# Optimization experiments

Measured on AMD Instinct MI355X. Metric: run time of the kernel, lower is better.

## Reference

```python
import jax, jax.numpy as jnp
import numpy as np

NUM_NODES = 100000
NUM_EDGES = 1600000
FEAT = 128
HID = 128
NUM_GRAPHS = 512


def setup_inputs() -> dict:
    key = jax.random.key(0)
    ks = jax.random.split(key, 8)
    x = jax.random.normal(ks[0], (NUM_NODES, FEAT), dtype=jnp.float32)
    edge_index = jax.random.randint(ks[1], (2, NUM_EDGES), 0, NUM_NODES, dtype=jnp.int64)
    batch = jnp.sort(jax.random.randint(ks[2], (NUM_NODES,), 0, NUM_GRAPHS, dtype=jnp.int64))
    # Glorot-ish init for weights (scale named for clarity)
    s1 = 1.0 / np.sqrt(FEAT)
    s2 = 1.0 / np.sqrt(HID)
    W1 = jax.random.normal(ks[3], (FEAT, HID), dtype=jnp.float32) * s1
    b1 = jnp.zeros((HID,), dtype=jnp.float32)
    W2 = jax.random.normal(ks[4], (HID, HID), dtype=jnp.float32) * s2
    b2 = jnp.zeros((HID,), dtype=jnp.float32)
    Wout = jax.random.normal(ks[5], (HID, 1), dtype=jnp.float32) * s2
    bout = jnp.zeros((1,), dtype=jnp.float32)
    return {"x": x, "edge_index": edge_index, "batch": batch,
            "W1": W1, "b1": b1, "W2": W2, "b2": b2, "Wout": Wout, "bout": bout}


def reference(x, edge_index, batch, W1, b1, W2, b2, Wout, bout):
    N = x.shape[0]
    # PyG GCNConv: add self-loops, symmetric normalization D^-1/2 (A+I) D^-1/2
    loops = jnp.arange(N, dtype=edge_index.dtype)
    src = jnp.concatenate([edge_index[0], loops])  # [E+N]
    dst = jnp.concatenate([edge_index[1], loops])  # [E+N]
    ones = jnp.ones_like(dst, dtype=x.dtype)
    deg = jax.ops.segment_sum(ones, dst, num_segments=N)  # in-degree incl. self-loop
    dinv = jnp.where(deg > 0, jax.lax.rsqrt(deg), 0.0)
    coeff = (dinv[src] * dinv[dst])[:, None]  # [E+N, 1]

    def gcn(h, W, b):
        h = h @ W                                       # [N, H] dense GEMM
        msg = h[src] * coeff                            # gather + scale
        agg = jax.ops.segment_sum(msg, dst, num_segments=N)  # scatter-add
        return agg + b

    h = jax.nn.relu(gcn(x, W1, b1))
    h = jax.nn.relu(gcn(h, W2, b2))

    # global_mean_pool over batch ids
    G = NUM_GRAPHS
    sums = jax.ops.segment_sum(h, batch, num_segments=G)
    cnts = jax.ops.segment_sum(jnp.ones((N,), dtype=h.dtype), batch, num_segments=G)
    pooled = sums / jnp.maximum(cnts, 1.0)[:, None]

    return pooled @ Wout + bout  # [G, 1]
```

## Files before the change

kernel.cpp:

```cpp
#include <hip/hip_runtime.h>
#include <hip/hip_bf16.h>
#include <hip/hip_fp16.h>

#define FEAT 128
#define PSLOTS 64
#define BSH 7
#define BNODES 128
#define BCAP 2560
#define NBIN 512

typedef _Float16 h8 __attribute__((ext_vector_type(8)));
typedef float f4 __attribute__((ext_vector_type(4)));
typedef float fx2 __attribute__((ext_vector_type(2)));


__device__ __forceinline__ void wt_body(const float* __restrict__ W1,
                                        const float* __restrict__ W2,
                                        __half* __restrict__ Wt1,
                                        __half* __restrict__ Wt2, int bid) {
    int t = bid * 256 + threadIdx.x;
    const float* W = (t < 8192) ? W1 : W2;
    __half* Wt     = (t < 8192) ? Wt1 : Wt2;
    int u = t & 8191;
    int n = u >> 6, k2 = (u & 63) * 2;
    float a = W[(size_t)k2 * 128 + n];
    float b = W[(size_t)(k2 + 1) * 128 + n];
    ((__half2*)Wt)[n * 64 + (k2 >> 1)] = __floats2half2_rn(a, b);
}

__device__ __forceinline__ void bin_body(const int* __restrict__ ei, int E, int chunk,
                                         int* __restrict__ cursor,
                                         unsigned* __restrict__ binned, int nb,
                                         int bid, int* smem) {
    int* hist = smem;
    int* base = smem + 1024;
    int start = bid * chunk;
    int end = start + chunk; if (end > E) end = E;
    bool vec4 = ((E & 3) == 0);
    int end4 = vec4 ? (start + ((end - start) & ~3)) : start;

    for (int i = threadIdx.x; i < nb; i += 256) hist[i] = 0;
    __syncthreads();
    for (int e = start + threadIdx.x * 4; e < end4; e += 1024) {
        int4 d4 = *(const int4*)(ei + E + e);
        atomicAdd(&hist[d4.x >> BSH], 1);
        atomicAdd(&hist[d4.y >> BSH], 1);
        atomicAdd(&hist[d4.z >> BSH], 1);
        atomicAdd(&hist[d4.w >> BSH], 1);
    }
    for (int e = end4 + threadIdx.x; e < end; e += 256)
        atomicAdd(&hist[ei[E + e] >> BSH], 1);
    __syncthreads();
    for (int i = threadIdx.x; i < nb; i += 256) {
        int h = hist[i];
        base[i] = h ? atomicAdd(&cursor[i], h) : 0;
    }
    __syncthreads();
    for (int e = start + threadIdx.x * 4; e < end4; e += 1024) {
        int4 s4 = *(const int4*)(ei + e);
        int4 d4 = *(const int4*)(ei + E + e);
        int sv[4] = {s4.x, s4.y, s4.z, s4.w};
        int dv[4] = {d4.x, d4.y, d4.z, d4.w};
#pragma unroll
        for (int j = 0; j < 4; ++j) {
            int b = dv[j] >> BSH;
            int pos = atomicAdd(&base[b], 1);
            if (pos < BCAP)
                binned[(size_t)b * BCAP + pos] =
                    (unsigned)sv[j] | ((unsigned)(dv[j] & (BNODES - 1)) << 17);
        }
    }
    for (int e = end4 + threadIdx.x; e < end; e += 256) {
        int s = ei[e];
        int d = ei[E + e];
        int b = d >> BSH;
        int pos = atomicAdd(&base[b], 1);
        if (pos < BCAP)
            binned[(size_t)b * BCAP + pos] =
                (unsigned)s | ((unsigned)(d & (BNODES - 1)) << 17);
    }
}

__global__ __launch_bounds__(256) void bin_wt(const int* __restrict__ ei, int E, int chunk,
                                              int* __restrict__ cursor,
                                              unsigned* __restrict__ binned, int nb,
                                              const float* __restrict__ W1,
                                              const float* __restrict__ W2,
                                              __half* __restrict__ Wt1,
                                              __half* __restrict__ Wt2) {
    __shared__ int smem[2048];
    if ((int)blockIdx.x < NBIN)
        bin_body(ei, E, chunk, cursor, binned, nb, blockIdx.x, smem);
    else
        wt_body(W1, W2, Wt1, Wt2, blockIdx.x - NBIN);
}


__device__ __forceinline__ void stage_wt(const __half* __restrict__ Wt, _Float16* Bs) {
    const float4* src = (const float4*)Wt;
    float4* dst = (float4*)Bs;
    for (int i = threadIdx.x; i < 2048; i += 256) {
        int n = i >> 4, ch = i & 15;
        dst[n * 16 + (ch ^ (n & 15))] = src[i];
    }
}

__device__ __forceinline__ void loadA(const __half* p, int quad, h8* a) {
#pragma unroll
    for (int ks = 0; ks < 4; ++ks)
        a[ks] = *(const h8*)(p + ks * 32 + quad * 8);
}
__device__ __forceinline__ void loadA(const float* p, int quad, h8* a) {
#pragma unroll
    for (int ks = 0; ks < 4; ++ks) {
        const float* q = p + ks * 32 + quad * 8;
        float4 f0 = *(const float4*)q;
        float4 f1 = *(const float4*)(q + 4);
        h8 v;
        v[0] = (_Float16)f0.x; v[1] = (_Float16)f0.y;
        v[2] = (_Float16)f0.z; v[3] = (_Float16)f0.w;
        v[4] = (_Float16)f1.x; v[5] = (_Float16)f1.y;
        v[6] = (_Float16)f1.z; v[7] = (_Float16)f1.w;
        a[ks] = v;
    }
}

template <typename TIN>
__device__ __forceinline__ void gemm_tile(const TIN* __restrict__ X, const _Float16* Bs,
                                          int rowb, int N, int m, int quad,
                                          f4 acc[2][8]) {
    h8 a[2][4];
#pragma unroll
    for (int rt = 0; rt < 2; ++rt) {
        int rA = rowb + rt * 64 + m; if (rA >= N) rA = N - 1;
        loadA(X + (size_t)rA * FEAT, quad, a[rt]);
    }
#pragma unroll
    for (int rt = 0; rt < 2; ++rt)
#pragma unroll
        for (int nt = 0; nt < 8; ++nt) acc[rt][nt] = (f4){0.f, 0.f, 0.f, 0.f};
#pragma unroll
    for (int nt = 0; nt < 8; ++nt) {
        const _Float16* bbase = Bs + (nt * 16 + m) * 128;
#pragma unroll
        for (int ks = 0; ks < 4; ++ks) {
            int ch = (ks * 4 + quad) ^ m;
            h8 bfrag = *(const h8*)(bbase + ch * 8);
            acc[0][nt] = __builtin_amdgcn_mfma_f32_16x16x32_f16(a[0][ks], bfrag, acc[0][nt], 0, 0, 0);
            acc[1][nt] = __builtin_amdgcn_mfma_f32_16x16x32_f16(a[1][ks], bfrag, acc[1][nt], 0, 0, 0);
        }
    }
}


__global__ __launch_bounds__(256) void k_build1(const unsigned* __restrict__ binned,
                                                const int* __restrict__ cursor,
                                                const float* __restrict__ X,
                                                const __half* __restrict__ Wt1,
                                                int N, int* __restrict__ deg,
                                                int* __restrict__ rowstart,
                                                int* __restrict__ meta,
                                                unsigned char* __restrict__ Y) {
    __shared__ __align__(16) _Float16 Bs[128 * 128];
    __shared__ int ld[256];
    __shared__ int sc[256];
    __shared__ int cur[256];
    int b = blockIdx.x;

    stage_wt(Wt1, Bs);

    int cnt = cursor[b]; if (cnt > BCAP) cnt = BCAP;
    int s = b * BCAP, e = s + cnt;
    ld[threadIdx.x] = 0;
    __syncthreads();
    for (int i = s + threadIdx.x; i < e; i += 256)
        atomicAdd(&ld[binned[i] >> 17], 1);
    __syncthreads();
    int d = ld[threadIdx.x];
    sc[threadIdx.x] = d;
    __syncthreads();
    for (int off = 1; off < 256; off <<= 1) {
        int t = (threadIdx.x >= off) ? sc[threadIdx.x - off] : 0;
        __syncthreads();
        sc[threadIdx.x] += t;
        __syncthreads();
    }
    int rs = s + sc[threadIdx.x] - d;
    cur[threadIdx.x] = rs;
    int v = (b << BSH) + threadIdx.x;
    if (threadIdx.x < BNODES && v < N) {
        deg[v] = d;
        rowstart[v] = rs;
    }
    __syncthreads();
    for (int i = s + threadIdx.x; i < e; i += 256) {
        unsigned p = binned[i];
        int src = (int)(p & 0x1FFFF);
        int drl = (int)(p >> 17);
        int pos = atomicAdd(&cur[drl], 1);
        meta[pos] = src << 7;
    }

    int lane = threadIdx.x & 63;
    int wave = threadIdx.x >> 6;
    int m = lane & 15;
    int quad = lane >> 4;
    int rowb = (b << BSH) + wave * 16;
    f4 acc[2][8];
    gemm_tile<float>(X, Bs, rowb, N, m, quad, acc);
#pragma unroll
    for (int rt = 0; rt < 2; ++rt)
#pragma unroll
    for (int r = 0; r < 4; ++r) {
        int row = rowb + rt * 64 + quad * 4 + r;
        if (row < N) {
            float scv = rsqrtf((float)ld[row & (BNODES - 1)] + 1.0f);
#pragma unroll
            for (int nt = 0; nt < 8; ++nt) {
                float val = scv * acc[rt][nt][r];
                int pk = __builtin_amdgcn_cvt_pk_fp8_f32(val, val, 0, false);
                Y[(size_t)row * FEAT + nt * 16 + m] = (unsigned char)(pk & 0xFF);
            }
        }
    }
}


__global__ __launch_bounds__(256) void gemm_mfma(const __half* __restrict__ X,
                                                 const __half* __restrict__ Wt,
                                                 unsigned char* __restrict__ Y,
                                                 const int* __restrict__ deg, int N) {
    __shared__ __align__(16) _Float16 Bs[128 * 128];
    stage_wt(Wt, Bs);
    __syncthreads();
    int lane = threadIdx.x & 63;
    int wave = threadIdx.x >> 6;
    int m = lane & 15;
    int quad = lane >> 4;
    int rowb = blockIdx.x * 128 + wave * 16;
    f4 acc[2][8];
    gemm_tile<__half>(X, Bs, rowb, N, m, quad, acc);
#pragma unroll
    for (int rt = 0; rt < 2; ++rt)
#pragma unroll
    for (int r = 0; r < 4; ++r) {
        int row = rowb + rt * 64 + quad * 4 + r;
        if (row < N) {
            float scv = rsqrtf((float)deg[row] + 1.0f);
#pragma unroll
            for (int nt = 0; nt < 8; ++nt) {
                float val = scv * acc[rt][nt][r];
                int pk = __builtin_amdgcn_cvt_pk_fp8_f32(val, val, 0, false);
                Y[(size_t)row * FEAT + nt * 16 + m] = (unsigned char)(pk & 0xFF);
            }
        }
    }
}


__device__ __forceinline__ void accum8(uint2 u, fx2* acc) {
    acc[0] += __builtin_amdgcn_cvt_pk_f32_fp8((int)u.x, false);
    acc[1] += __builtin_amdgcn_cvt_pk_f32_fp8((int)u.x, true);
    acc[2] += __builtin_amdgcn_cvt_pk_f32_fp8((int)u.y, false);
    acc[3] += __builtin_amdgcn_cvt_pk_f32_fp8((int)u.y, true);
}

template <bool POOL>
__global__ __launch_bounds__(256) void agg_relu(const unsigned char* __restrict__ Y,
                                                const int* __restrict__ rowstart,
                                                const int* __restrict__ degc,
                                                const int* __restrict__ meta,
                                                const float* __restrict__ bias,
                                                __half* __restrict__ H, int N, int zoff,
                                                const float* __restrict__ Wout,
                                                const int* __restrict__ batch,
                                                float* __restrict__ gsum, int G) {
    int wid  = (blockIdx.x * 256 + threadIdx.x) >> 6;
    int lane = threadIdx.x & 63;
    if (wid >= N) return;
    int v = wid;
    int g = lane >> 4;
    int c = lane & 15;
    int cb = c * 8;
    const char* Ycb = (const char*)Y + cb;

    fx2 acc[4];
#pragma unroll
    for (int k = 0; k < 4; ++k) acc[k] = (fx2){0.f, 0.f};

    {
        int so = (g == 0) ? (v << 7) : zoff;
        uint2 u = *(const uint2*)(Ycb + so);
        accum8(u, acc);
    }

    int base = rowstart[v];
    int n = degc[v];
    int g4 = g * 4;
    for (int i0 = 0; i0 < n; i0 += 16) {
        int o[4];
#pragma unroll
        for (int j = 0; j < 4; ++j) {
            int idx = i0 + g4 + j;
            int mj = meta[base + idx];
            o[j] = (idx < n) ? mj : zoff;
        }
        uint2 u[4];
#pragma unroll
        for (int j = 0; j < 4; ++j)
            u[j] = *(const uint2*)(Ycb + o[j]);
#pragma unroll
        for (int j = 0; j < 4; ++j) accum8(u[j], acc);
    }

#pragma unroll
    for (int k = 0; k < 4; ++k) {
        fx2 t;
        t[0] = __shfl_xor(acc[k][0], 16);
        t[1] = __shfl_xor(acc[k][1], 16);
        acc[k] += t;
        t[0] = __shfl_xor(acc[k][0], 32);
        t[1] = __shfl_xor(acc[k][1], 32);
        acc[k] += t;
    }
    float dv = rsqrtf((float)n + 1.0f);

    if (POOL) {
        const float4* bp = (const float4*)(bias + cb);
        float4 b0 = bp[0], b1 = bp[1];
        const float4* wp = (const float4*)(Wout + cb);
        float4 w0 = wp[0], w1 = wp[1];
        float h0 = fmaxf(dv * acc[0][0] + b0.x, 0.f);
        float h1 = fmaxf(dv * acc[0][1] + b0.y, 0.f);
        float h2 = fmaxf(dv * acc[1][0] + b0.z, 0.f);
        float h3 = fmaxf(dv * acc[1][1] + b0.w, 0.f);
        float h4 = fmaxf(dv * acc[2][0] + b1.x, 0.f);
        float h5 = fmaxf(dv * acc[2][1] + b1.y, 0.f);
        float h6 = fmaxf(dv * acc[3][0] + b1.z, 0.f);
        float h7 = fmaxf(dv * acc[3][1] + b1.w, 0.f);
        float s = h0 * w0.x + h1 * w0.y + h2 * w0.z + h3 * w0.w
                + h4 * w1.x + h5 * w1.y + h6 * w1.z + h7 * w1.w;
        if (g == 0) {
            s += __shfl_xor(s, 1);
            s += __shfl_xor(s, 2);
            s += __shfl_xor(s, 4);
            s += __shfl_xor(s, 8);
            if (lane == 0) {
                int slot = blockIdx.x & (PSLOTS - 1);
                atomicAdd(&gsum[slot * G + batch[v]], s);
            }
        }
    } else {
        fx2 av;
        if (g == 0)      av = acc[0];
        else if (g == 1) av = acc[1];
        else if (g == 2) av = acc[2];
        else             av = acc[3];
        float2 bb = *(const float2*)(bias + cb + g * 2);
        float hx = fmaxf(dv * av[0] + bb.x, 0.f);
        float hy = fmaxf(dv * av[1] + bb.y, 0.f);
        *(__half2*)(H + (size_t)v * FEAT + cb + g * 2) = __floats2half2_rn(hx, hy);
    }
}


__global__ __launch_bounds__(256) void k_head(const float* __restrict__ gsum,
                                              const int* __restrict__ batch, int N, int G,
                                              const float* __restrict__ bout,
                                              float* __restrict__ out) {
    int g = blockIdx.x * 256 + threadIdx.x;
    if (g >= G) return;
    float s = 0.f;
#pragma unroll 8
    for (int k = 0; k < PSLOTS; ++k) s += gsum[k * G + g];
    int lo = 0, hi = N;
    while (lo < hi) { int mid = (lo + hi) >> 1; if (batch[mid] < g) lo = mid + 1; else hi = mid; }
    int start = lo;
    lo = start; hi = N;
    while (lo < hi) { int mid = (lo + hi) >> 1; if (batch[mid] < g + 1) lo = mid + 1; else hi = mid; }
    int cnt = lo - start;
    out[g] = s / (float)(cnt > 0 ? cnt : 1) + bout[0];
}


extern "C" void kernel_launch(void* const* d_in, const int* in_sizes, int n_in,
                              void* d_out, int out_size, void* d_ws, size_t ws_size,
                              hipStream_t stream) {
    const float* x    = (const float*)d_in[0];
    const int*   ei   = (const int*)d_in[1];
    const int*   batch= (const int*)d_in[2];
    const float* W1   = (const float*)d_in[3];
    const float* b1   = (const float*)d_in[4];
    const float* W2   = (const float*)d_in[5];
    const float* b2   = (const float*)d_in[6];
    const float* Wout = (const float*)d_in[7];
    const float* bout = (const float*)d_in[8];

    int N = in_sizes[0] / FEAT;
    int E = in_sizes[1] / 2;
    int G = out_size;
    int nb = (N + BNODES - 1) >> BSH;

    char* ws = (char*)d_ws;
    size_t off = 0;
    auto alloc = [&](size_t bytes) -> void* {
        void* p = ws + off;
        off += (bytes + 255) & ~(size_t)255;
        return p;
    };
    unsigned char* bufY = (unsigned char*)alloc((size_t)N * FEAT);
    __half* bufH     = (__half*)alloc((size_t)N * FEAT * 2);
    __half* Wt1      = (__half*)alloc((size_t)FEAT * FEAT * 2);
    __half* Wt2      = (__half*)alloc((size_t)FEAT * FEAT * 2);
    size_t zbytes    = 256 + (size_t)PSLOTS * G * 4 + (size_t)nb * 4;
    char*  zr        = (char*)alloc(zbytes);
    unsigned char* padrow = (unsigned char*)zr;
    float* gsum      = (float*)(zr + 256);
    int*   cursor    = (int*)(gsum + (size_t)PSLOTS * G);
    int    zoff      = (int)((char*)padrow - (char*)bufY);
    int*   deg       = (int*)alloc((size_t)N * 4);
    int*   rowstart  = (int*)alloc((size_t)N * 4);
    unsigned* binned = (unsigned*)alloc((size_t)nb * BCAP * 4);
    int*   meta      = (int*)alloc(((size_t)nb * BCAP + 64) * 4);

    int gemm_grid = (N + 127) / 128;
    int agg_grid  = (N + 3) / 4;
    int chunkB = (((E + NBIN - 1) / NBIN) + 3) & ~3;

    hipMemsetAsync(zr, 0, zbytes, stream);
    bin_wt<<<NBIN + 64, 256, 0, stream>>>(ei, E, chunkB, cursor, binned, nb,
                                          W1, W2, Wt1, Wt2);
    k_build1<<<nb, 256, 0, stream>>>(binned, cursor, x, Wt1, N, deg, rowstart, meta, bufY);
    agg_relu<false><<<agg_grid, 256, 0, stream>>>(bufY, rowstart, deg, meta, b1, bufH, N, zoff,
                                                  nullptr, nullptr, nullptr, 0);
    gemm_mfma<<<gemm_grid, 256, 0, stream>>>(bufH, Wt2, bufY, deg, N);
    agg_relu<true><<<agg_grid, 256, 0, stream>>>(bufY, rowstart, deg, meta, b2, nullptr, N, zoff,
                                                 Wout, batch, gsum, G);
    k_head<<<(G + 255) / 256, 256, 0, stream>>>(gsum, batch, N, G, bout, (float*)d_out);
}
```

Baseline: 277.7 us.

## Run layer-1 GEMM concurrently with edge binning, apply source norm in aggregation

The first-layer GEMM no longer waits for the degree computation. It writes unscaled fp8 rows and runs in the same launch as the edge-binning blocks, so the dense and sparse setup work overlap. The source-side normalization moves into the first aggregation as a per-edge weight gathered from a new dinv array. The memset and weight transpose are folded into one init kernel. The cost is an extra per-edge dinv gather and multiply in layer 1, plus the fp8 quantization now applying to unscaled values.

Result: slower. 286.1 us (+3.1%).

```diff
diff --git a/kernel.cpp b/kernel.cpp
--- a/kernel.cpp
+++ b/kernel.cpp
@@ -28,6 +28,18 @@
     ((__half2*)Wt)[n * 64 + (k2 >> 1)] = __floats2half2_rn(a, b);
 }
 
+
+__global__ __launch_bounds__(256) void k_init(const float* __restrict__ W1,
+                                              const float* __restrict__ W2,
+                                              __half* __restrict__ Wt1,
+                                              __half* __restrict__ Wt2,
+                                              uint4* __restrict__ zr, int zwords) {
+    if ((int)blockIdx.x < 64) { wt_body(W1, W2, Wt1, Wt2, blockIdx.x); return; }
+    int t = (blockIdx.x - 64) * 256 + threadIdx.x;
+    int stride = (gridDim.x - 64) * 256;
+    for (int i = t; i < zwords; i += stride) zr[i] = make_uint4(0, 0, 0, 0);
+}
+
 __device__ __forceinline__ void bin_body(const int* __restrict__ ei, int E, int chunk,
                                          int* __restrict__ cursor,
                                          unsigned* __restrict__ binned, int nb,
@@ -81,20 +93,6 @@
     }
 }
 
-__global__ __launch_bounds__(256) void bin_wt(const int* __restrict__ ei, int E, int chunk,
-                                              int* __restrict__ cursor,
-                                              unsigned* __restrict__ binned, int nb,
-                                              const float* __restrict__ W1,
-                                              const float* __restrict__ W2,
-                                              __half* __restrict__ Wt1,
-                                              __half* __restrict__ Wt2) {
-    __shared__ int smem[2048];
-    if ((int)blockIdx.x < NBIN)
-        bin_body(ei, E, chunk, cursor, binned, nb, blockIdx.x, smem);
-    else
-        wt_body(W1, W2, Wt1, Wt2, blockIdx.x - NBIN);
-}
-
 
 __device__ __forceinline__ void stage_wt(const __half* __restrict__ Wt, _Float16* Bs) {
     const float4* src = (const float4*)Wt;
@@ -152,69 +150,17 @@
     }
 }
 
-
-__global__ __launch_bounds__(256) void k_build1(const unsigned* __restrict__ binned,
-                                                const int* __restrict__ cursor,
-                                                const float* __restrict__ X,
-                                                const __half* __restrict__ Wt1,
-                                                int N, int* __restrict__ deg,
-                                                int* __restrict__ rowstart,
-                                                int* __restrict__ meta,
-                                                unsigned char* __restrict__ Y) {
-    __shared__ __align__(16) _Float16 Bs[128 * 128];
-    __shared__ int ld[256];
-    __shared__ int sc[256];
-    __shared__ int cur[256];
-    int b = blockIdx.x;
-
-    stage_wt(Wt1, Bs);
-
-    int cnt = cursor[b]; if (cnt > BCAP) cnt = BCAP;
-    int s = b * BCAP, e = s + cnt;
-    ld[threadIdx.x] = 0;
-    __syncthreads();
-    for (int i = s + threadIdx.x; i < e; i += 256)
-        atomicAdd(&ld[binned[i] >> 17], 1);
-    __syncthreads();
-    int d = ld[threadIdx.x];
-    sc[threadIdx.x] = d;
-    __syncthreads();
-    for (int off = 1; off < 256; off <<= 1) {
-        int t = (threadIdx.x >= off) ? sc[threadIdx.x - off] : 0;
-        __syncthreads();
-        sc[threadIdx.x] += t;
-        __syncthreads();
-    }
-    int rs = s + sc[threadIdx.x] - d;
-    cur[threadIdx.x] = rs;
-    int v = (b << BSH) + threadIdx.x;
-    if (threadIdx.x < BNODES && v < N) {
-        deg[v] = d;
-        rowstart[v] = rs;
-    }
-    __syncthreads();
-    for (int i = s + threadIdx.x; i < e; i += 256) {
-        unsigned p = binned[i];
-        int src = (int)(p & 0x1FFFF);
-        int drl = (int)(p >> 17);
-        int pos = atomicAdd(&cur[drl], 1);
-        meta[pos] = src << 7;
-    }
-
-    int lane = threadIdx.x & 63;
-    int wave = threadIdx.x >> 6;
-    int m = lane & 15;
-    int quad = lane >> 4;
-    int rowb = (b << BSH) + wave * 16;
-    f4 acc[2][8];
-    gemm_tile<float>(X, Bs, rowb, N, m, quad, acc);
+template <bool SCALED>
+__device__ __forceinline__ void gemm_store(f4 acc[2][8], unsigned char* __restrict__ Y,
+                                           const int* __restrict__ deg,
+                                           int rowb, int N, int m, int quad) {
 #pragma unroll
     for (int rt = 0; rt < 2; ++rt)
 #pragma unroll
     for (int r = 0; r < 4; ++r) {
         int row = rowb + rt * 64 + quad * 4 + r;
         if (row < N) {
-            float scv = rsqrtf((float)ld[row & (BNODES - 1)] + 1.0f);
+            float scv = SCALED ? rsqrtf((float)deg[row] + 1.0f) : 1.0f;
 #pragma unroll
             for (int nt = 0; nt < 8; ++nt) {
                 float val = scv * acc[rt][nt][r];
@@ -222,6 +168,32 @@
                 Y[(size_t)row * FEAT + nt * 16 + m] = (unsigned char)(pk & 0xFF);
             }
         }
+    }
+}
+
+
+__global__ __launch_bounds__(256) void gemm_bin(const float* __restrict__ X,
+                                                const __half* __restrict__ Wt1,
+                                                unsigned char* __restrict__ Y, int N,
+                                                int gemm_grid,
+                                                const int* __restrict__ ei, int E, int chunk,
+                                                int* __restrict__ cursor,
+                                                unsigned* __restrict__ binned, int nb) {
+    __shared__ __align__(16) char smem[32768];
+    if ((int)blockIdx.x < gemm_grid) {
+        _Float16* Bs = (_Float16*)smem;
+        stage_wt(Wt1, Bs);
+        __syncthreads();
+        int lane = threadIdx.x & 63;
+        int wave = threadIdx.x >> 6;
+        int m = lane & 15;
+        int quad = lane >> 4;
+        int rowb = blockIdx.x * 128 + wave * 16;
+        f4 acc[2][8];
+        gemm_tile<float>(X, Bs, rowb, N, m, quad, acc);
+        gemm_store<false>(acc, Y, nullptr, rowb, N, m, quad);
+    } else {
+        bin_body(ei, E, chunk, cursor, binned, nb, blockIdx.x - gemm_grid, (int*)smem);
     }
 }
 
@@ -240,20 +212,51 @@
     int rowb = blockIdx.x * 128 + wave * 16;
     f4 acc[2][8];
     gemm_tile<__half>(X, Bs, rowb, N, m, quad, acc);
-#pragma unroll
-    for (int rt = 0; rt < 2; ++rt)
-#pragma unroll
-    for (int r = 0; r < 4; ++r) {
-        int row = rowb + rt * 64 + quad * 4 + r;
-        if (row < N) {
-            float scv = rsqrtf((float)deg[row] + 1.0f);
-#pragma unroll
-            for (int nt = 0; nt < 8; ++nt) {
-                float val = scv * acc[rt][nt][r];
-                int pk = __builtin_amdgcn_cvt_pk_fp8_f32(val, val, 0, false);
-                Y[(size_t)row * FEAT + nt * 16 + m] = (unsigned char)(pk & 0xFF);
-            }
-        }
+    gemm_store<true>(acc, Y, deg, rowb, N, m, quad);
+}
+
+
+__global__ __launch_bounds__(256) void k_build(const unsigned* __restrict__ binned,
+                                               const int* __restrict__ cursor,
+                                               int N, int* __restrict__ deg,
+                                               int* __restrict__ rowstart,
+                                               float* __restrict__ dinv,
+                                               int* __restrict__ meta) {
+    __shared__ int ld[256];
+    __shared__ int sc[256];
+    __shared__ int cur[256];
+    int b = blockIdx.x;
+    int cnt = cursor[b]; if (cnt > BCAP) cnt = BCAP;
+    int s = b * BCAP, e = s + cnt;
+    ld[threadIdx.x] = 0;
+    __syncthreads();
+    for (int i = s + threadIdx.x; i < e; i += 256)
+        atomicAdd(&ld[binned[i] >> 17], 1);
+    __syncthreads();
+    int d = ld[threadIdx.x];
+    sc[threadIdx.x] = d;
+    __syncthreads();
+    for (int off = 1; off < 256; off <<= 1) {
+        int t = (threadIdx.x >= off) ? sc[threadIdx.x - off] : 0;
+        __syncthreads();
+        sc[threadIdx.x] += t;
+        __syncthreads();
+    }
+    int rs = s + sc[threadIdx.x] - d;
+    cur[threadIdx.x] = rs;
+    int v = (b << BSH) + threadIdx.x;
+    if (threadIdx.x < BNODES && v < N) {
+        deg[v] = d;
+        rowstart[v] = rs;
+        dinv[v] = rsqrtf((float)d + 1.0f);
+    }
+    __syncthreads();
+    for (int i = s + threadIdx.x; i < e; i += 256) {
+        unsigned p = binned[i];
+        int src = (int)(p & 0x1FFFF);
+        int drl = (int)(p >> 17);
+        int pos = atomicAdd(&cur[drl], 1);
+        meta[pos] = src << 7;
     }
 }
 
@@ -264,11 +267,19 @@
     acc[2] += __builtin_amdgcn_cvt_pk_f32_fp8((int)u.y, false);
     acc[3] += __builtin_amdgcn_cvt_pk_f32_fp8((int)u.y, true);
 }
-
-template <bool POOL>
+__device__ __forceinline__ void accum8w(uint2 u, float cf, fx2* acc) {
+    fx2 c = (fx2){cf, cf};
+    acc[0] += c * __builtin_amdgcn_cvt_pk_f32_fp8((int)u.x, false);
+    acc[1] += c * __builtin_amdgcn_cvt_pk_f32_fp8((int)u.x, true);
+    acc[2] += c * __builtin_amdgcn_cvt_pk_f32_fp8((int)u.y, false);
+    acc[3] += c * __builtin_amdgcn_cvt_pk_f32_fp8((int)u.y, true);
+}
+
+template <bool POOL, bool WEIGHTED>
 __global__ __launch_bounds__(256) void agg_relu(const unsigned char* __restrict__ Y,
                                                 const int* __restrict__ rowstart,
                                                 const int* __restrict__ degc,
+                                                const float* __restrict__ dinv,
                                                 const int* __restrict__ meta,
                                                 const float* __restrict__ bias,
                                                 __half* __restrict__ H, int N, int zoff,
@@ -283,6 +294,7 @@
     int c = lane & 15;
     int cb = c * 8;
     const char* Ycb = (const char*)Y + cb;
+    float dv = WEIGHTED ? dinv[v] : 0.f;
 
     fx2 acc[4];
 #pragma unroll
@@ -291,7 +303,8 @@
     {
         int so = (g == 0) ? (v << 7) : zoff;
         uint2 u = *(const uint2*)(Ycb + so);
-        accum8(u, acc);
+        if (WEIGHTED) accum8w(u, dv, acc);
+        else          accum8(u, acc);
     }
 
     int base = rowstart[v];
@@ -299,18 +312,27 @@
     int g4 = g * 4;
     for (int i0 = 0; i0 < n; i0 += 16) {
         int o[4];
+        float cf[4];
 #pragma unroll
         for (int j = 0; j < 4; ++j) {
             int idx = i0 + g4 + j;
             int mj = meta[base + idx];
-            o[j] = (idx < n) ? mj : zoff;
+            bool ok = idx < n;
+            o[j] = ok ? mj : zoff;
+            if (WEIGHTED) {
+                cf[j] = 0.f;
+                if (ok) cf[j] = dinv[mj >> 7];
+            }
         }
         uint2 u[4];
 #pragma unroll
         for (int j = 0; j < 4; ++j)
             u[j] = *(const uint2*)(Ycb + o[j]);
 #pragma unroll
-        for (int j = 0; j < 4; ++j) accum8(u[j], acc);
+        for (int j = 0; j < 4; ++j) {
+            if (WEIGHTED) accum8w(u[j], cf[j], acc);
+            else          accum8(u[j], acc);
+        }
     }
 
 #pragma unroll
@@ -323,7 +345,7 @@
         t[1] = __shfl_xor(acc[k][1], 32);
         acc[k] += t;
     }
-    float dv = rsqrtf((float)n + 1.0f);
+    if (!WEIGHTED) dv = rsqrtf((float)n + 1.0f);
 
     if (POOL) {
         const float4* bp = (const float4*)(bias + cb);
@@ -420,21 +442,25 @@
     int    zoff      = (int)((char*)padrow - (char*)bufY);
     int*   deg       = (int*)alloc((size_t)N * 4);
     int*   rowstart  = (int*)alloc((size_t)N * 4);
+    float* dinv      = (float*)alloc((size_t)N * 4);
     unsigned* binned = (unsigned*)alloc((size_t)nb * BCAP * 4);
     int*   meta      = (int*)alloc(((size_t)nb * BCAP + 64) * 4);
 
     int gemm_grid = (N + 127) / 128;
     int agg_grid  = (N + 3) / 4;
     int chunkB = (((E + NBIN - 1) / NBIN) + 3) & ~3;
-
-    hipMemsetAsync(zr, 0, zbytes, stream);
-    bin_wt<<<NBIN + 64, 256, 0, stream>>>(ei, E, chunkB, cursor, binned, nb,
-                                          W1, W2, Wt1, Wt2);
-    k_build1<<<nb, 256, 0, stream>>>(binned, cursor, x, Wt1, N, deg, rowstart, meta, bufY);
-    agg_relu<false><<<agg_grid, 256, 0, stream>>>(bufY, rowstart, deg, meta, b1, bufH, N, zoff,
-                                                  nullptr, nullptr, nullptr, 0);
+    int zwords = (int)((zbytes + 15) / 16);
+
+    k_init<<<224, 256, 0, stream>>>(W1, W2, Wt1, Wt2, (uint4*)zr, zwords);
+    gemm_bin<<<gemm_grid + NBIN, 256, 0, stream>>>(x, Wt1, bufY, N, gemm_grid,
+                                                   ei, E, chunkB, cursor, binned, nb);
+    k_build<<<nb, 256, 0, stream>>>(binned, cursor, N, deg, rowstart, dinv, meta);
+    agg_relu<false, true><<<agg_grid, 256, 0, stream>>>(bufY, rowstart, deg, dinv, meta,
+                                                        b1, bufH, N, zoff,
+                                                        nullptr, nullptr, nullptr, 0);
     gemm_mfma<<<gemm_grid, 256, 0, stream>>>(bufH, Wt2, bufY, deg, N);
-    agg_relu<true><<<agg_grid, 256, 0, stream>>>(bufY, rowstart, deg, meta, b2, nullptr, N, zoff,
-                                                 Wout, batch, gsum, G);
+    agg_relu<true, false><<<agg_grid, 256, 0, stream>>>(bufY, rowstart, deg, dinv, meta,
+                                                        b2, nullptr, N, zoff,
+                                                        Wout, batch, gsum, G);
     k_head<<<(G + 255) / 256, 256, 0, stream>>>(gsum, batch, N, G, bout, (float*)d_out);
 }
```

## Fuse binning and build into persistent kernel with grid barrier; fold head into pool

Applied to the files above, without the earlier changes.

Merges the edge-binning/weight-transpose kernel and the per-bin CSR build + first GEMM into one persistent kernel of 768 blocks that synchronise through a global atomic spin barrier. The gsum zeroing also moves into that kernel, and the final head computation is folded into the last block of the pooling aggregation via a done counter. The aim is to cut launch gaps and the memset. In exchange it relies on all 768 blocks being co-resident for the spin barrier to be safe, and it serialises the head into a single block.

New measurement: 1.081 ms. 3.89x slower.

```diff
diff --git a/kernel.cpp b/kernel.cpp
--- a/kernel.cpp
+++ b/kernel.cpp
@@ -7,7 +7,8 @@
 #define BSH 7
 #define BNODES 128
 #define BCAP 2560
-#define NBIN 512
+#define NBIN 704
+#define KG_GRID 768
 
 typedef _Float16 h8 __attribute__((ext_vector_type(8)));
 typedef float f4 __attribute__((ext_vector_type(4)));
@@ -81,20 +82,6 @@
     }
 }
 
-__global__ __launch_bounds__(256) void bin_wt(const int* __restrict__ ei, int E, int chunk,
-                                              int* __restrict__ cursor,
-                                              unsigned* __restrict__ binned, int nb,
-                                              const float* __restrict__ W1,
-                                              const float* __restrict__ W2,
-                                              __half* __restrict__ Wt1,
-                                              __half* __restrict__ Wt2) {
-    __shared__ int smem[2048];
-    if ((int)blockIdx.x < NBIN)
-        bin_body(ei, E, chunk, cursor, binned, nb, blockIdx.x, smem);
-    else
-        wt_body(W1, W2, Wt1, Wt2, blockIdx.x - NBIN);
-}
-
 
 __device__ __forceinline__ void stage_wt(const __half* __restrict__ Wt, _Float16* Bs) {
     const float4* src = (const float4*)Wt;
@@ -153,20 +140,15 @@
 }
 
 
-__global__ __launch_bounds__(256) void k_build1(const unsigned* __restrict__ binned,
-                                                const int* __restrict__ cursor,
-                                                const float* __restrict__ X,
-                                                const __half* __restrict__ Wt1,
-                                                int N, int* __restrict__ deg,
-                                                int* __restrict__ rowstart,
-                                                int* __restrict__ meta,
-                                                unsigned char* __restrict__ Y) {
-    __shared__ __align__(16) _Float16 Bs[128 * 128];
-    __shared__ int ld[256];
-    __shared__ int sc[256];
-    __shared__ int cur[256];
-    int b = blockIdx.x;
-
+__device__ __forceinline__ void build_body(int b, const unsigned* __restrict__ binned,
+                                           const int* __restrict__ cursor,
+                                           const float* __restrict__ X,
+                                           const __half* __restrict__ Wt1,
+                                           int N, int* __restrict__ deg,
+                                           int* __restrict__ rowstart,
+                                           int* __restrict__ meta,
+                                           unsigned char* __restrict__ Y,
+                                           _Float16* Bs, int* ld, int* sc, int* cur) {
     stage_wt(Wt1, Bs);
 
     int cnt = cursor[b]; if (cnt > BCAP) cnt = BCAP;
@@ -226,6 +208,50 @@
 }
 
 
+__global__ __launch_bounds__(256, 4) void k_graph(const int* __restrict__ ei, int E, int chunk,
+                                                  int* __restrict__ cursor,
+                                                  unsigned* __restrict__ binned, int nb,
+                                                  const float* __restrict__ W1,
+                                                  const float* __restrict__ W2,
+                                                  __half* __restrict__ Wt1,
+                                                  __half* __restrict__ Wt2,
+                                                  uint4* __restrict__ zr4, int zwords,
+                                                  const float* __restrict__ X, int N,
+                                                  int* __restrict__ deg,
+                                                  int* __restrict__ rowstart,
+                                                  int* __restrict__ meta,
+                                                  unsigned char* __restrict__ Y,
+                                                  int* __restrict__ done1) {
+    __shared__ __align__(16) char smem[35840];
+    int u = blockIdx.x;
+    if (u < NBIN) {
+        bin_body(ei, E, chunk, cursor, binned, nb, u, (int*)smem);
+    } else {
+        int w = u - NBIN;
+        wt_body(W1, W2, Wt1, Wt2, w);
+        int i = w * 129 + (int)threadIdx.x;
+        if (threadIdx.x < 129 && i < zwords) zr4[i] = make_uint4(0, 0, 0, 0);
+    }
+    __syncthreads();
+    if (threadIdx.x == 0) {
+        __threadfence();
+        __hip_atomic_fetch_add(done1, 1, __ATOMIC_RELEASE, __HIP_MEMORY_SCOPE_AGENT);
+        while (__hip_atomic_load(done1, __ATOMIC_ACQUIRE, __HIP_MEMORY_SCOPE_AGENT) < (int)gridDim.x)
+            __builtin_amdgcn_s_sleep(2);
+        __threadfence();
+    }
+    __syncthreads();
+    _Float16* Bs = (_Float16*)smem;
+    int* ld = (int*)(smem + 32768);
+    int* sc = ld + 256;
+    int* cur = sc + 256;
+    for (int b = blockIdx.x; b < nb; b += gridDim.x) {
+        __syncthreads();
+        build_body(b, binned, cursor, X, Wt1, N, deg, rowstart, meta, Y, Bs, ld, sc, cur);
+    }
+}
+
+
 __global__ __launch_bounds__(256) void gemm_mfma(const __half* __restrict__ X,
                                                  const __half* __restrict__ Wt,
                                                  unsigned char* __restrict__ Y,
@@ -254,6 +280,26 @@
                 Y[(size_t)row * FEAT + nt * 16 + m] = (unsigned char)(pk & 0xFF);
             }
         }
+    }
+}
+
+
+__device__ void head_body(float* __restrict__ gsum, const int* __restrict__ batch,
+                          int N, int G, const float* __restrict__ bout,
+                          float* __restrict__ out) {
+    float bo = bout[0];
+    for (int g = threadIdx.x; g < G; g += 256) {
+        float s = 0.f;
+#pragma unroll 8
+        for (int k = 0; k < PSLOTS; ++k)
+            s += __hip_atomic_load(&gsum[k * G + g], __ATOMIC_RELAXED, __HIP_MEMORY_SCOPE_AGENT);
+        int lo = 0, hi = N;
+        while (lo < hi) { int mid = (lo + hi) >> 1; if (batch[mid] < g) lo = mid + 1; else hi = mid; }
+        int start = lo;
+        lo = start; hi = N;
+        while (lo < hi) { int mid = (lo + hi) >> 1; if (batch[mid] < g + 1) lo = mid + 1; else hi = mid; }
+        int cnt = lo - start;
+        out[g] = s / (float)(cnt > 0 ? cnt : 1) + bo;
     }
 }
 
@@ -274,112 +320,109 @@
                                                 __half* __restrict__ H, int N, int zoff,
                                                 const float* __restrict__ Wout,
                                                 const int* __restrict__ batch,
-                                                float* __restrict__ gsum, int G) {
+                                                float* __restrict__ gsum, int G,
+                                                int* __restrict__ done2,
+                                                const float* __restrict__ bout,
+                                                float* __restrict__ out) {
     int wid  = (blockIdx.x * 256 + threadIdx.x) >> 6;
     int lane = threadIdx.x & 63;
-    if (wid >= N) return;
-    int v = wid;
-    int g = lane >> 4;
-    int c = lane & 15;
-    int cb = c * 8;
-    const char* Ycb = (const char*)Y + cb;
-
-    fx2 acc[4];
-#pragma unroll
-    for (int k = 0; k < 4; ++k) acc[k] = (fx2){0.f, 0.f};
-
-    {
-        int so = (g == 0) ? (v << 7) : zoff;
-        uint2 u = *(const uint2*)(Ycb + so);
-        accum8(u, acc);
-    }
-
-    int base = rowstart[v];
-    int n = degc[v];
-    int g4 = g * 4;
-    for (int i0 = 0; i0 < n; i0 += 16) {
-        int o[4];
-#pragma unroll
-        for (int j = 0; j < 4; ++j) {
-            int idx = i0 + g4 + j;
-            int mj = meta[base + idx];
-            o[j] = (idx < n) ? mj : zoff;
-        }
-        uint2 u[4];
-#pragma unroll
-        for (int j = 0; j < 4; ++j)
-            u[j] = *(const uint2*)(Ycb + o[j]);
-#pragma unroll
-        for (int j = 0; j < 4; ++j) accum8(u[j], acc);
-    }
-
-#pragma unroll
-    for (int k = 0; k < 4; ++k) {
-        fx2 t;
-        t[0] = __shfl_xor(acc[k][0], 16);
-        t[1] = __shfl_xor(acc[k][1], 16);
-        acc[k] += t;
-        t[0] = __shfl_xor(acc[k][0], 32);
-        t[1] = __shfl_xor(acc[k][1], 32);
-        acc[k] += t;
-    }
-    float dv = rsqrtf((float)n + 1.0f);
-
+    bool active = wid < N;
+    if (active) {
+        int v = wid;
+        int g = lane >> 4;
+        int c = lane & 15;
+        int cb = c * 8;
+        const char* Ycb = (const char*)Y + cb;
+
+        fx2 acc[4];
+#pragma unroll
+        for (int k = 0; k < 4; ++k) acc[k] = (fx2){0.f, 0.f};
+
+        {
+            int so = (g == 0) ? (v << 7) : zoff;
+            uint2 u = *(const uint2*)(Ycb + so);
+            accum8(u, acc);
+        }
+
+        int base = rowstart[v];
+        int n = degc[v];
+        int g4 = g * 4;
+        for (int i0 = 0; i0 < n; i0 += 16) {
+            int o[4];
+#pragma unroll
+            for (int j = 0; j < 4; ++j) {
+                int idx = i0 + g4 + j;
+                int mj = meta[base + idx];
+                o[j] = (idx < n) ? mj : zoff;
+            }
+            uint2 u[4];
+#pragma unroll
+            for (int j = 0; j < 4; ++j)
+                u[j] = *(const uint2*)(Ycb + o[j]);
+#pragma unroll
+            for (int j = 0; j < 4; ++j) accum8(u[j], acc);
+        }
+
+#pragma unroll
+        for (int k = 0; k < 4; ++k) {
+            fx2 t;
+            t[0] = __shfl_xor(acc[k][0], 16);
+            t[1] = __shfl_xor(acc[k][1], 16);
+            acc[k] += t;
+            t[0] = __shfl_xor(acc[k][0], 32);
+            t[1] = __shfl_xor(acc[k][1], 32);
+            acc[k] += t;
+        }
+        float dv = rsqrtf((float)n + 1.0f);
+
+        if (POOL) {
+            const float4* bp = (const float4*)(bias + cb);
+            float4 b0 = bp[0], b1 = bp[1];
+            const float4* wp = (const float4*)(Wout + cb);
+            float4 w0 = wp[0], w1 = wp[1];
+            float h0 = fmaxf(dv * acc[0][0] + b0.x, 0.f);
+            float h1 = fmaxf(dv * acc[0][1] + b0.y, 0.f);
+            float h2 = fmaxf(dv * acc[1][0] + b0.z, 0.f);
+            float h3 = fmaxf(dv * acc[1][1] + b0.w, 0.f);
+            float h4 = fmaxf(dv * acc[2][0] + b1.x, 0.f);
+            float h5 = fmaxf(dv * acc[2][1] + b1.y, 0.f);
+            float h6 = fmaxf(dv * acc[3][0] + b1.z, 0.f);
+            float h7 = fmaxf(dv * acc[3][1] + b1.w, 0.f);
+            float s = h0 * w0.x + h1 * w0.y + h2 * w0.z + h3 * w0.w
+                    + h4 * w1.x + h5 * w1.y + h6 * w1.z + h7 * w1.w;
+            if (g == 0) {
+                s += __shfl_xor(s, 1);
+                s += __shfl_xor(s, 2);
+                s += __shfl_xor(s, 4);
+                s += __shfl_xor(s, 8);
+                if (lane == 0) {
+                    int slot = blockIdx.x & (PSLOTS - 1);
+                    atomicAdd(&gsum[slot * G + batch[wid]], s);
+                }
+            }
+        } else {
+            fx2 av;
+            if (g == 0)      av = acc[0];
+            else if (g == 1) av = acc[1];
+            else if (g == 2) av = acc[2];
+            else             av = acc[3];
+            float2 bb = *(const float2*)(bias + cb + g * 2);
+            float hx = fmaxf(dv * av[0] + bb.x, 0.f);
+            float hy = fmaxf(dv * av[1] + bb.y, 0.f);
+            *(__half2*)(H + (size_t)v * FEAT + cb + g * 2) = __floats2half2_rn(hx, hy);
+        }
+    }
     if (POOL) {
-        const float4* bp = (const float4*)(bias + cb);
-        float4 b0 = bp[0], b1 = bp[1];
-        const float4* wp = (const float4*)(Wout + cb);
-        float4 w0 = wp[0], w1 = wp[1];
-        float h0 = fmaxf(dv * acc[0][0] + b0.x, 0.f);
-        float h1 = fmaxf(dv * acc[0][1] + b0.y, 0.f);
-        float h2 = fmaxf(dv * acc[1][0] + b0.z, 0.f);
-        float h3 = fmaxf(dv * acc[1][1] + b0.w, 0.f);
-        float h4 = fmaxf(dv * acc[2][0] + b1.x, 0.f);
-        float h5 = fmaxf(dv * acc[2][1] + b1.y, 0.f);
-        float h6 = fmaxf(dv * acc[3][0] + b1.z, 0.f);
-        float h7 = fmaxf(dv * acc[3][1] + b1.w, 0.f);
-        float s = h0 * w0.x + h1 * w0.y + h2 * w0.z + h3 * w0.w
-                + h4 * w1.x + h5 * w1.y + h6 * w1.z + h7 * w1.w;
-        if (g == 0) {
-            s += __shfl_xor(s, 1);
-            s += __shfl_xor(s, 2);
-            s += __shfl_xor(s, 4);
-            s += __shfl_xor(s, 8);
-            if (lane == 0) {
-                int slot = blockIdx.x & (PSLOTS - 1);
-                atomicAdd(&gsum[slot * G + batch[v]], s);
-            }
-        }
-    } else {
-        fx2 av;
-        if (g == 0)      av = acc[0];
-        else if (g == 1) av = acc[1];
-        else if (g == 2) av = acc[2];
-        else             av = acc[3];
-        float2 bb = *(const float2*)(bias + cb + g * 2);
-        float hx = fmaxf(dv * av[0] + bb.x, 0.f);
-        float hy = fmaxf(dv * av[1] + bb.y, 0.f);
-        *(__half2*)(H + (size_t)v * FEAT + cb + g * 2) = __floats2half2_rn(hx, hy);
-    }
-}
-
-
-__global__ __launch_bounds__(256) void k_head(const float* __restrict__ gsum,
-                                              const int* __restrict__ batch, int N, int G,
-                                              const float* __restrict__ bout,
-                                              float* __restrict__ out) {
-    int g = blockIdx.x * 256 + threadIdx.x;
-    if (g >= G) return;
-    float s = 0.f;
-#pragma unroll 8
-    for (int k = 0; k < PSLOTS; ++k) s += gsum[k * G + g];
-    int lo = 0, hi = N;
-    while (lo < hi) { int mid = (lo + hi) >> 1; if (batch[mid] < g) lo = mid + 1; else hi = mid; }
-    int start = lo;
-    lo = start; hi = N;
-    while (lo < hi) { int mid = (lo + hi) >> 1; if (batch[mid] < g + 1) lo = mid + 1; else hi = mid; }
-    int cnt = lo - start;
-    out[g] = s / (float)(cnt > 0 ? cnt : 1) + bout[0];
+        __syncthreads();
+        __shared__ int isLast;
+        if (threadIdx.x == 0) {
+            int old = __hip_atomic_fetch_add(done2, 1, __ATOMIC_ACQ_REL,
+                                             __HIP_MEMORY_SCOPE_AGENT);
+            isLast = (old == (int)gridDim.x - 1);
+        }
+        __syncthreads();
+        if (isLast) head_body(gsum, batch, N, G, bout, out);
+    }
 }
 
 
@@ -412,12 +455,14 @@
     __half* bufH     = (__half*)alloc((size_t)N * FEAT * 2);
     __half* Wt1      = (__half*)alloc((size_t)FEAT * FEAT * 2);
     __half* Wt2      = (__half*)alloc((size_t)FEAT * FEAT * 2);
-    size_t zbytes    = 256 + (size_t)PSLOTS * G * 4 + (size_t)nb * 4;
+    size_t zbytes    = 256 + (size_t)PSLOTS * G * 4;
     char*  zr        = (char*)alloc(zbytes);
     unsigned char* padrow = (unsigned char*)zr;
     float* gsum      = (float*)(zr + 256);
-    int*   cursor    = (int*)(gsum + (size_t)PSLOTS * G);
     int    zoff      = (int)((char*)padrow - (char*)bufY);
+    int*   cursor    = (int*)alloc((size_t)nb * 4 + 32);
+    int*   done1     = cursor + nb;
+    int*   done2     = done1 + 1;
     int*   deg       = (int*)alloc((size_t)N * 4);
     int*   rowstart  = (int*)alloc((size_t)N * 4);
     unsigned* binned = (unsigned*)alloc((size_t)nb * BCAP * 4);
@@ -426,15 +471,17 @@
     int gemm_grid = (N + 127) / 128;
     int agg_grid  = (N + 3) / 4;
     int chunkB = (((E + NBIN - 1) / NBIN) + 3) & ~3;
-
-    hipMemsetAsync(zr, 0, zbytes, stream);
-    bin_wt<<<NBIN + 64, 256, 0, stream>>>(ei, E, chunkB, cursor, binned, nb,
-                                          W1, W2, Wt1, Wt2);
-    k_build1<<<nb, 256, 0, stream>>>(binned, cursor, x, Wt1, N, deg, rowstart, meta, bufY);
-    agg_relu<false><<<agg_grid, 256, 0, stream>>>(bufY, rowstart, deg, meta, b1, bufH, N, zoff,
-                                                  nullptr, nullptr, nullptr, 0);
+    int zwords = (int)((zbytes + 15) / 16);
+
+    hipMemsetAsync(cursor, 0, (size_t)nb * 4 + 32, stream);
+    k_graph<<<KG_GRID, 256, 0, stream>>>(ei, E, chunkB, cursor, binned, nb,
+                                         W1, W2, Wt1, Wt2, (uint4*)zr, zwords,
+                                         x, N, deg, rowstart, meta, bufY, done1);
+    agg_relu<false><<<agg_grid, 256, 0, stream>>>(bufY, rowstart, deg, meta, b1, bufH,
+                                                  N, zoff, nullptr, nullptr, nullptr, 0,
+                                                  nullptr, nullptr, nullptr);
     gemm_mfma<<<gemm_grid, 256, 0, stream>>>(bufH, Wt2, bufY, deg, N);
-    agg_relu<true><<<agg_grid, 256, 0, stream>>>(bufY, rowstart, deg, meta, b2, nullptr, N, zoff,
-                                                 Wout, batch, gsum, G);
-    k_head<<<(G + 255) / 256, 256, 0, stream>>>(gsum, batch, N, G, bout, (float*)d_out);
-}
+    agg_relu<true><<<agg_grid, 256, 0, stream>>>(bufY, rowstart, deg, meta, b2, nullptr,
+                                                 N, zoff, Wout, batch, gsum, G,
+                                                 done2, bout, (float*)d_out);
+}
```
